# Kernel tuning notes

Measured on AMD Instinct MI355X. Metric: run time of the kernel, lower is better.

The kernel has to match this reference:

```python
import math
import jax, jax.numpy as jnp
import numpy as np

B, S, IN_DIM, D_MODEL, L, T_Y = 16, 512, 64, 64, 32, 256
T_X = T_Y + L - 1
RIDGE = 0.01
THRESH = 0.005


def _pos_encoding(seq_len, d):
    pos = jnp.arange(seq_len, dtype=jnp.float32)[:, None]
    div = jnp.exp(jnp.arange(0, d, 2, dtype=jnp.float32) * (-(math.log(10000.0) / d)))
    ang = pos * div  # [S, d/2]
    pe = jnp.zeros((seq_len, d), dtype=jnp.float32)
    pe = pe.at[:, 0::2].set(jnp.sin(ang)).at[:, 1::2].set(jnp.cos(ang))
    return pe


def _layernorm(h, gamma, beta, eps=1e-5):
    mu = jnp.mean(h, axis=-1, keepdims=True)
    var = jnp.mean((h - mu) ** 2, axis=-1, keepdims=True)
    return (h - mu) * jax.lax.rsqrt(var + eps) * gamma + beta


def setup_inputs() -> dict:
    key = jax.random.key(0)
    ks = jax.random.split(key, 8)
    return {
        "fps": jax.random.normal(ks[0], (B, S, IN_DIM), dtype=jnp.float32),
        "x": jax.random.normal(ks[1], (B, S, T_X), dtype=jnp.float32),
        "y": jax.random.normal(ks[2], (B, S, T_Y), dtype=jnp.float32),
        "sample_steps": jax.random.randint(ks[3], (5,), 10, S),
        "W1": jax.random.normal(ks[4], (IN_DIM, 256), dtype=jnp.float32) / math.sqrt(IN_DIM),
        "b1": jnp.zeros((256,), dtype=jnp.float32),
        "gamma": jnp.ones((256,), dtype=jnp.float32),
        "beta": jnp.zeros((256,), dtype=jnp.float32),
        "W2": jax.random.normal(ks[5], (256, D_MODEL), dtype=jnp.float32) / math.sqrt(256.0),
        "b2": jnp.zeros((D_MODEL,), dtype=jnp.float32),
        "Wq": jax.random.normal(ks[6], (D_MODEL, D_MODEL), dtype=jnp.float32) / math.sqrt(D_MODEL),
        "bq": jnp.zeros((D_MODEL,), dtype=jnp.float32),
        "Wk": jax.random.normal(ks[7], (D_MODEL, D_MODEL), dtype=jnp.float32) / math.sqrt(D_MODEL),
        "bk": jnp.zeros((D_MODEL,), dtype=jnp.float32),
    }


def reference(fps, x, y, sample_steps, W1, b1, gamma, beta, W2, b2, Wq, bq, Wk, bk):
    batch, seq_len, _ = fps.shape
    d = Wq.shape[0]
    t_y = y.shape[-1]
    filt = x.shape[-1] - t_y + 1  # L

    # encoder: Linear -> LayerNorm -> Tanh -> Linear -> Tanh
    h = _layernorm(fps @ W1 + b1, gamma, beta)
    e_orig = jnp.tanh(jnp.tanh(h) @ W2 + b2)  # [B,S,d]
    e = e_orig + 0.05 * _pos_encoding(seq_len, d)[None]

    q = e @ Wq + bq
    k = e @ Wk + bk
    scores = jnp.einsum('bsd,btd->bst', q, k) / math.sqrt(d)
    causal = jnp.triu(jnp.ones((seq_len, seq_len), dtype=bool), 1)
    scores = jnp.where(causal[None], -1e9, scores)
    alpha = jax.nn.softmax(scores * 2.0, axis=-1)  # [B,S,S]

    # sliding windows: X[b,s] = unfold(x[b,s], L, 1)[:T_y] -> [T_y, L]
    win = jnp.arange(t_y)[:, None] + jnp.arange(filt)[None, :]
    X = x[:, :, win]  # [B,S,T_y,L]

    # per-source gram / cross contributions
    G = jnp.einsum('bstl,bstm->bslm', X, X)  # [B,S,L,L]
    C = jnp.einsum('bstl,bst->bsl', X, y)    # [B,S,L]

    w = alpha[:, sample_steps, :]            # [B,T,S]
    wm = jnp.where(w > THRESH, w, 0.0)

    gram = jnp.einsum('bts,bslm->btlm', wm, G) + RIDGE * jnp.eye(filt, dtype=x.dtype)
    cross = jnp.einsum('bts,bsl->btl', wm, C)
    wt_hat = jnp.linalg.solve(gram, cross[..., None])[..., 0]  # [B,T,L]

    Xt = X[:, sample_steps]  # [B,T,T_y,L]
    yt = y[:, sample_steps]  # [B,T,T_y]
    pred = jnp.einsum('btkl,btl->btk', Xt, wt_hat)
    loss_bt = jnp.mean((yt - pred) ** 2, axis=-1)  # [B,T]

    valid = jnp.any(wm > 0.0, axis=-1)  # [B,T]
    total = jnp.sum(jnp.where(valid, loss_bt, 0.0))
    n = jnp.maximum(jnp.sum(valid.astype(jnp.int32)), 1)
    loss = total / n
    return loss, alpha, e_orig
```

## Files before the change

### kernel.cpp

```cpp
#include <hip/hip_runtime.h>
#include <hip/hip_bf16.h>
#include <math.h>

#define BB 16
#define SS 512
#define INDIM 64
#define DMODEL 64
#define HID 256
#define FILT 32
#define TYY 256
#define TXX 287
#define NT 5
#define RIDGEF 0.01f
#define THRESHF 0.005f

__global__ __launch_bounds__(256) void k_mlp(
    const float* __restrict__ fps, const float* __restrict__ W1, const float* __restrict__ b1,
    const float* __restrict__ gamma, const float* __restrict__ beta,
    const float* __restrict__ W2, const float* __restrict__ b2,
    const float* __restrict__ Wq, const float* __restrict__ bq,
    const float* __restrict__ Wk, const float* __restrict__ bk,
    float* __restrict__ e_out, float* __restrict__ q_out, float* __restrict__ kT_out)
{
    const int row0 = blockIdx.x << 2;
    const int tid = threadIdx.x;
    const int wid = tid >> 6, lane = tid & 63;

    __shared__ float fr[4][INDIM];
    __shared__ float th4[4][HID];
    __shared__ float ee4[4][DMODEL];
    __shared__ float part4[4][4][DMODEL];
    __shared__ float partk4[4][4][DMODEL];
    __shared__ float wred[4][4][2];

    { int r = tid >> 6, i = tid & 63;
      fr[r][i] = fps[(row0 + r) * INDIM + i]; }
    __syncthreads();

    float h[4];
    float b1v = b1[tid];
    #pragma unroll
    for (int r = 0; r < 4; ++r) h[r] = b1v;
    for (int i = 0; i < INDIM; ++i) {
        float w = W1[i * HID + tid];
        #pragma unroll
        for (int r = 0; r < 4; ++r) h[r] = fmaf(fr[r][i], w, h[r]);
    }

    float s1[4], s2[4];
    #pragma unroll
    for (int r = 0; r < 4; ++r) { s1[r] = h[r]; s2[r] = h[r] * h[r]; }
    #pragma unroll
    for (int off = 1; off < 64; off <<= 1) {
        #pragma unroll
        for (int r = 0; r < 4; ++r) {
            s1[r] += __shfl_xor(s1[r], off);
            s2[r] += __shfl_xor(s2[r], off);
        }
    }
    if (lane == 0) {
        #pragma unroll
        for (int r = 0; r < 4; ++r) { wred[wid][r][0] = s1[r]; wred[wid][r][1] = s2[r]; }
    }
    __syncthreads();
    float gm = gamma[tid], bt = beta[tid];
    #pragma unroll
    for (int r = 0; r < 4; ++r) {
        float t1 = wred[0][r][0] + wred[1][r][0] + wred[2][r][0] + wred[3][r][0];
        float t2 = wred[0][r][1] + wred[1][r][1] + wred[2][r][1] + wred[3][r][1];
        float mu = t1 * (1.0f / HID);
        float var = t2 * (1.0f / HID) - mu * mu;
        float hn = (h[r] - mu) * rsqrtf(var + 1e-5f) * gm + bt;
        th4[r][tid] = tanhf(hn);
    }
    __syncthreads();

    { int p = tid >> 6, j = tid & 63;
      float acc[4] = {0.f, 0.f, 0.f, 0.f};
      for (int i = p * 64; i < p * 64 + 64; ++i) {
          float w = W2[i * DMODEL + j];
          #pragma unroll
          for (int r = 0; r < 4; ++r) acc[r] = fmaf(th4[r][i], w, acc[r]);
      }
      #pragma unroll
      for (int r = 0; r < 4; ++r) part4[p][r][j] = acc[r];
    }
    __syncthreads();
    { int r = tid >> 6, j = tid & 63;
      float e = part4[0][r][j] + part4[1][r][j] + part4[2][r][j] + part4[3][r][j] + b2[j];
      float eo = tanhf(e);
      int row = row0 + r;
      int s = row & (SS - 1);
      e_out[(size_t)row * DMODEL + j] = eo;
      float div = expf(-(float)(j & ~1) * 0.14391156831212787f);
      float ang = (float)s * div;
      float pe = (j & 1) ? cosf(ang) : sinf(ang);
      ee4[r][j] = eo + 0.05f * pe;
    }
    __syncthreads();
    { int p = tid >> 6, j = tid & 63;
      float aq[4] = {0.f,0.f,0.f,0.f}, ak[4] = {0.f,0.f,0.f,0.f};
      for (int i = p * 16; i < p * 16 + 16; ++i) {
          float wqv = Wq[i * DMODEL + j];
          float wkv = Wk[i * DMODEL + j];
          #pragma unroll
          for (int r = 0; r < 4; ++r) {
              aq[r] = fmaf(ee4[r][i], wqv, aq[r]);
              ak[r] = fmaf(ee4[r][i], wkv, ak[r]);
          }
      }
      #pragma unroll
      for (int r = 0; r < 4; ++r) { part4[p][r][j] = aq[r]; partk4[p][r][j] = ak[r]; }
    }
    __syncthreads();
    { int r = tid >> 6, j = tid & 63;
      float qv = part4[0][r][j] + part4[1][r][j] + part4[2][r][j] + part4[3][r][j] + bq[j];
      float kv = partk4[0][r][j] + partk4[1][r][j] + partk4[2][r][j] + partk4[3][r][j] + bk[j];
      int row = row0 + r;
      int b = row >> 9, s = row & (SS - 1);
      q_out[(size_t)row * DMODEL + j] = qv;
      kT_out[(size_t)(b * DMODEL + j) * SS + s] = kv;
    }
}

__global__ __launch_bounds__(256) void k_attn(
    const float* __restrict__ q, const float* __restrict__ kT,
    float* __restrict__ alpha)
{
    const int blk = blockIdx.x;
    const int b = blk >> 7;
    const int t0 = (blk & 127) << 2;
    const int t3 = t0 + 3;
    const int tid = threadIdx.x;
    const int wave = tid >> 6, lane = tid & 63;

    __shared__ float qt[4 * DMODEL];
    __shared__ float redm[4][4];

    qt[tid] = q[(size_t)(b * SS + t0 + (tid >> 6)) * DMODEL + (tid & 63)];
    __syncthreads();

    const float* kTb = kT + (size_t)b * DMODEL * SS;
    const int s0 = tid, s1 = tid + 256;
    float a0[4] = {0,0,0,0}, a1[4] = {0,0,0,0};
    if (s1 <= t3) {
        for (int d = 0; d < DMODEL; ++d) {
            float k0 = kTb[d * SS + s0];
            float k1 = kTb[d * SS + s1];
            #pragma unroll
            for (int r = 0; r < 4; ++r) {
                float qv = qt[r * DMODEL + d];
                a0[r] = fmaf(qv, k0, a0[r]);
                a1[r] = fmaf(qv, k1, a1[r]);
            }
        }
    } else if (s0 <= t3) {
        for (int d = 0; d < DMODEL; ++d) {
            float k0 = kTb[d * SS + s0];
            #pragma unroll
            for (int r = 0; r < 4; ++r) a0[r] = fmaf(qt[r * DMODEL + d], k0, a0[r]);
        }
    }
    float lg0[4], lg1[4];
    #pragma unroll
    for (int r = 0; r < 4; ++r) {
        int tr = t0 + r;
        lg0[r] = (s0 <= tr) ? 0.25f * a0[r] : -INFINITY;
        lg1[r] = (s1 <= tr) ? 0.25f * a1[r] : -INFINITY;
    }
    float mr[4];
    #pragma unroll
    for (int r = 0; r < 4; ++r) {
        float m = fmaxf(lg0[r], lg1[r]);
        #pragma unroll
        for (int off = 32; off > 0; off >>= 1) m = fmaxf(m, __shfl_xor(m, off));
        if (lane == 0) redm[r][wave] = m;
    }
    __syncthreads();
    #pragma unroll
    for (int r = 0; r < 4; ++r)
        mr[r] = fmaxf(fmaxf(redm[r][0], redm[r][1]), fmaxf(redm[r][2], redm[r][3]));
    __syncthreads();
    float ex0[4], ex1[4], sr[4];
    #pragma unroll
    for (int r = 0; r < 4; ++r) {
        ex0[r] = expf(lg0[r] - mr[r]);
        ex1[r] = expf(lg1[r] - mr[r]);
        float sm = ex0[r] + ex1[r];
        #pragma unroll
        for (int off = 32; off > 0; off >>= 1) sm += __shfl_xor(sm, off);
        if (lane == 0) redm[r][wave] = sm;
    }
    __syncthreads();
    #pragma unroll
    for (int r = 0; r < 4; ++r)
        sr[r] = redm[r][0] + redm[r][1] + redm[r][2] + redm[r][3];
    #pragma unroll
    for (int r = 0; r < 4; ++r) {
        float inv = 1.0f / sr[r];
        size_t base = (size_t)(b * SS + t0 + r) * SS;
        alpha[base + s0] = ex0[r] * inv;
        alpha[base + s1] = ex1[r] * inv;
    }
}

__global__ __launch_bounds__(256) void k_gpart(
    const float* __restrict__ x, const float* __restrict__ y,
    const int* __restrict__ steps, const float* __restrict__ alpha,
    float* __restrict__ part, int C, int CS)
{
    const int b = blockIdx.x / C;
    const int chunk = blockIdx.x % C;
    const int tid = threadIdx.x;
    const int lane = tid & 63, wid = tid >> 6;

    __shared__ __align__(16) float xs[288];
    __shared__ __align__(16) float ys[256];
    __shared__ float Gs[1056];
    __shared__ float crossL[32];
    __shared__ float wv[NT * 64];
    __shared__ int sl[64];
    __shared__ int nselS;
    __shared__ int stS[NT];
    __shared__ float redA[4][33];
    __shared__ float redB[4][33];

    if (tid < NT) stS[tid] = steps[tid];
    if (tid < 32) Gs[tid * 33 + 32] = 0.f;
    __syncthreads();

    for (int idx = tid; idx < NT * CS; idx += 256) {
        int t = idx / CS, si = idx % CS;
        float a = alpha[(size_t)(b * SS + stS[t]) * SS + chunk * CS + si];
        wv[t * 64 + si] = (a > THRESHF) ? a : 0.f;
    }
    __syncthreads();
    if (tid == 0) {
        int c = 0;
        for (int si = 0; si < CS; ++si) {
            float m = wv[si] + wv[64 + si] + wv[128 + si] + wv[192 + si] + wv[256 + si];
            if (m > 0.f) sl[c++] = si;
        }
        nselS = c;
    }
    __syncthreads();
    const int nsel = nselS;

    float acc[NT][5];
    #pragma unroll
    for (int t = 0; t < NT; ++t) {
        #pragma unroll
        for (int r = 0; r < 5; ++r) acc[t][r] = 0.f;
    }

    float rx0 = 0.f, rx1 = 0.f, ry = 0.f;
    if (nsel > 0) {
        int sg = chunk * CS + sl[0];
        const float* xr = x + (size_t)(b * SS + sg) * TXX;
        const float* yr = y + (size_t)(b * SS + sg) * TYY;
        rx0 = xr[tid];
        if (tid < 31) rx1 = xr[256 + tid];
        ry = yr[tid];
    }

    for (int i = 0; i < nsel; ++i) {
        xs[tid] = rx0;
        if (tid < 31) xs[256 + tid] = rx1;
        ys[tid] = ry;
        const int sl_cur = sl[i];
        __syncthreads();

        if (i + 1 < nsel) {
            int sg = chunk * CS + sl[i + 1];
            const float* xr = x + (size_t)(b * SS + sg) * TXX;
            const float* yr = y + (size_t)(b * SS + sg) * TYY;
            rx0 = xr[tid];
            if (tid < 31) rx1 = xr[256 + tid];
            ry = yr[tid];
        }

        { int l = tid & 31, p = tid >> 5;
          const float4* xk4 = (const float4*)(xs + (p << 5));
          const float4* yk4 = (const float4*)(ys + (p << 5));
          float c = 0.f, a = 0.f;
          #pragma unroll
          for (int j = 0; j < 8; ++j) {
              float4 xk = xk4[j];
              float4 yk = yk4[j];
              int kb = (p << 5) + (j << 2);
              float x0 = xs[kb + l],     x1 = xs[kb + 1 + l];
              float x2 = xs[kb + 2 + l], x3 = xs[kb + 3 + l];
              c = fmaf(x0, yk.x, c); a = fmaf(xk.x, x0, a);
              c = fmaf(x1, yk.y, c); a = fmaf(xk.y, x1, a);
              c = fmaf(x2, yk.z, c); a = fmaf(xk.z, x2, a);
              c = fmaf(x3, yk.w, c); a = fmaf(xk.w, x3, a);
          }
          c += __shfl_xor(c, 32);
          a += __shfl_xor(a, 32);
          if (lane < 32) { redA[wid][l] = c; redB[wid][l] = a; }
        }
        __syncthreads();

        if (tid < 32)
            crossL[tid] = redA[0][tid] + redA[1][tid] + redA[2][tid] + redA[3][tid];

        { int jj = lane & 31;
          #pragma unroll
          for (int pass = 0; pass < 4; ++pass) {
              int dd = 2 * (wid + 4 * pass) + (lane >> 5);
              float g0 = redB[0][dd] + redB[1][dd] + redB[2][dd] + redB[3][dd];
              float dlt = 0.f;
              if (jj > 0 && jj + dd < 32)
                  dlt = xs[jj + 255] * xs[jj + 255 + dd]
                      - xs[jj - 1] * xs[jj - 1 + dd];
              #pragma unroll
              for (int off = 1; off < 32; off <<= 1) {
                  float tsh = __shfl_up(dlt, off, 32);
                  if (jj >= off) dlt += tsh;
              }
              if (jj + dd < 32) {
                  float gval = g0 + dlt;
                  Gs[jj * 33 + jj + dd] = gval;
                  Gs[(jj + dd) * 33 + jj] = gval;
              }
          }
        }
        __syncthreads();

        { float g0 = Gs[tid], g1 = Gs[tid + 256], g2 = Gs[tid + 512], g3 = Gs[tid + 768];
          float g4 = (tid < 32) ? Gs[1024 + tid]
                   : ((tid < 64) ? crossL[tid - 32] : 0.f);
          #pragma unroll
          for (int t = 0; t < NT; ++t) {
              float w = wv[t * 64 + sl_cur];
              if (w > 0.f) {
                  acc[t][0] = fmaf(w, g0, acc[t][0]);
                  acc[t][1] = fmaf(w, g1, acc[t][1]);
                  acc[t][2] = fmaf(w, g2, acc[t][2]);
                  acc[t][3] = fmaf(w, g3, acc[t][3]);
                  acc[t][4] = fmaf(w, g4, acc[t][4]);
              }
          }
        }
    }

    #pragma unroll
    for (int t = 0; t < NT; ++t) {
        size_t base = (size_t)((b * NT + t) * C + chunk) * 1088;
        #pragma unroll
        for (int r = 0; r < 4; ++r) part[base + tid + 256 * r] = acc[t][r];
        if (tid < 64) part[base + 1024 + tid] = acc[t][4];
    }
}

__global__ __launch_bounds__(256) void k_solve2(
    const float* __restrict__ x, const float* __restrict__ y,
    const int* __restrict__ steps, const float* __restrict__ alpha,
    const float* __restrict__ part,
    float* __restrict__ lossbt, int* __restrict__ valid, int C)
{
    const int g = blockIdx.x;
    const int b = g / NT, t = g % NT;
    const int tid = threadIdx.x;

    __shared__ float Af[1056];
    __shared__ float zs[FILT];
    __shared__ float wt[FILT];
    __shared__ float xsr[TXX + 1];
    __shared__ float red[256];
    __shared__ int step_s;
    __shared__ int anyv;

    if (tid == 0) { step_s = steps[t]; anyv = 0; }
    __syncthreads();

    float a0 = 0.f, a1 = 0.f, a2 = 0.f, a3 = 0.f, a4 = 0.f;
    for (int ch = 0; ch < C; ++ch) {
        const float* pp = part + (size_t)(g * C + ch) * 1088;
        a0 += pp[tid];
        a1 += pp[tid + 256];
        a2 += pp[tid + 512];
        a3 += pp[tid + 768];
        if (tid < 64) a4 += pp[tid + 1024];
    }
    Af[tid] = a0; Af[tid + 256] = a1; Af[tid + 512] = a2; Af[tid + 768] = a3;
    if (tid < 32) Af[1024 + tid] = a4;
    else if (tid < 64) zs[tid - 32] = a4;

    { const float* arow = alpha + (size_t)(b * SS + step_s) * SS;
      if (arow[tid] > THRESHF || arow[tid + 256] > THRESHF) anyv = 1; }
    __syncthreads();
    if (tid < 32) Af[tid * 33 + tid] += RIDGEF;
    __syncthreads();

    if (tid < 32) {
        float a[32];
        #pragma unroll
        for (int j = 0; j < 32; ++j) a[j] = Af[tid * 33 + j];
        #pragma unroll
        for (int k = 0; k < 32; ++k) {
            float akk = __shfl(a[k], k);
            float dk = sqrtf(akk);
            float ck = a[k] / dk;
            if (tid >= k) a[k] = ck;
            #pragma unroll
            for (int m = k + 1; m < 32; ++m) {
                float cm = __shfl(ck, m);
                if (tid >= m) a[m] = fmaf(-ck, cm, a[m]);
            }
        }
        #pragma unroll
        for (int j = 0; j < 32; ++j)
            if (j <= tid) Af[tid * 33 + j] = a[j];

        float zl = zs[tid];
        #pragma unroll
        for (int k = 0; k < 32; ++k) {
            float akk = __shfl(a[k], k);
            float zk = __shfl(zl, k) / akk;
            if (tid == k) zl = zk;
            else if (tid > k) zl = fmaf(-a[k], zk, zl);
        }
        #pragma unroll
        for (int k = 31; k >= 0; --k) {
            float akk = __shfl(a[k], k);
            float wk = __shfl(zl, k) / akk;
            if (tid == k) zl = wk;
            else if (tid < k) zl = fmaf(-Af[k * 33 + tid], wk, zl);
        }
        wt[tid] = zl;
    }
    __syncthreads();

    const int sstep = step_s;
    const float* xrow = x + (size_t)(b * SS + sstep) * TXX;
    for (int i = tid; i < TXX; i += 256) xsr[i] = xrow[i];
    __syncthreads();
    float pk = 0.f;
    #pragma unroll
    for (int l = 0; l < FILT; ++l) pk = fmaf(xsr[tid + l], wt[l], pk);
    float d = y[(size_t)(b * SS + sstep) * TYY + tid] - pk;
    red[tid] = d * d;
    __syncthreads();
    for (int off = 128; off > 0; off >>= 1) {
        if (tid < off) red[tid] += red[tid + off];
        __syncthreads();
    }
    if (tid == 0) {
        lossbt[g] = red[0] * (1.0f / TYY);
        valid[g] = anyv;
    }
}

__global__ __launch_bounds__(128) void k_final(
    const float* __restrict__ lossbt, const int* __restrict__ valid,
    float* __restrict__ out0)
{
    __shared__ float rs[128];
    __shared__ int rc[128];
    int tid = threadIdx.x;
    float v = 0.f; int c = 0;
    if (tid < BB * NT && valid[tid]) { v = lossbt[tid]; c = 1; }
    rs[tid] = v; rc[tid] = c;
    __syncthreads();
    for (int off = 64; off > 0; off >>= 1) {
        if (tid < off) { rs[tid] += rs[tid + off]; rc[tid] += rc[tid + off]; }
        __syncthreads();
    }
    if (tid == 0) {
        int n = rc[0] > 0 ? rc[0] : 1;
        out0[0] = rs[0] / (float)n;
    }
}

extern "C" void kernel_launch(void* const* d_in, const int* in_sizes, int n_in,
                              void* d_out, int out_size, void* d_ws, size_t ws_size,
                              hipStream_t stream)
{
    const float* fps  = (const float*)d_in[0];
    const float* x    = (const float*)d_in[1];
    const float* y    = (const float*)d_in[2];
    const int* steps  = (const int*)d_in[3];
    const float* W1   = (const float*)d_in[4];
    const float* b1   = (const float*)d_in[5];
    const float* gamma= (const float*)d_in[6];
    const float* beta = (const float*)d_in[7];
    const float* W2   = (const float*)d_in[8];
    const float* b2   = (const float*)d_in[9];
    const float* Wq   = (const float*)d_in[10];
    const float* bq   = (const float*)d_in[11];
    const float* Wk   = (const float*)d_in[12];
    const float* bk   = (const float*)d_in[13];

    float* out   = (float*)d_out;
    float* alpha = out + 1;
    float* e_out = out + 1 + (size_t)BB * SS * SS;

    float* lossbt = (float*)d_ws;
    int*   valid  = (int*)(lossbt + 128);
    float* shreg  = (float*)d_ws + 256;
    float* q      = shreg;
    float* kT     = q + (size_t)BB * SS * DMODEL;
    float* part   = shreg;

    size_t avail_f = (ws_size > 1024) ? (ws_size / 4 - 256) : 0;
    int C = 64;
    while (C > 8 && (size_t)(BB * NT) * C * 1088 > avail_f) C >>= 1;
    int CS = SS / C;

    hipLaunchKernelGGL(k_mlp, dim3(BB * SS / 4), dim3(256), 0, stream,
                       fps, W1, b1, gamma, beta, W2, b2, Wq, bq, Wk, bk,
                       e_out, q, kT);
    hipLaunchKernelGGL(k_attn, dim3(BB * (SS / 4)), dim3(256), 0, stream,
                       q, kT, alpha);
    hipLaunchKernelGGL(k_gpart, dim3(BB * C), dim3(256), 0, stream,
                       x, y, steps, alpha, part, C, CS);
    hipLaunchKernelGGL(k_solve2, dim3(BB * NT), dim3(256), 0, stream,
                       x, y, steps, alpha, part, lossbt, valid, C);
    hipLaunchKernelGGL(k_final, dim3(1), dim3(128), 0, stream, lossbt, valid, out);
}
```

Before: 209.9 us.

## Split chunk reduction into parallel kernel and process 8 rows per MLP block

Adds a k_reduce kernel that sums the per-chunk gram/cross partials across 400 blocks into a compact gram buffer. Previously the 80 k_solve2 blocks each did this summation serially. k_mlp now handles 8 rows per block, reusing each W1 load across more rows and halving the block count; the second-layer and projection stages run in two halves of 4 rows. The changes add a kernel launch, an extra workspace buffer, and more registers in k_mlp.

```diff
diff --git a/kernel.cpp b/kernel.cpp
--- a/kernel.cpp
+++ b/kernel.cpp
@@ -22,50 +22,51 @@
     const float* __restrict__ Wk, const float* __restrict__ bk,
     float* __restrict__ e_out, float* __restrict__ q_out, float* __restrict__ kT_out)
 {
-    const int row0 = blockIdx.x << 2;
+    const int row0 = blockIdx.x << 3;
     const int tid = threadIdx.x;
     const int wid = tid >> 6, lane = tid & 63;
 
-    __shared__ float fr[4][INDIM];
-    __shared__ float th4[4][HID];
+    __shared__ float fr[8][INDIM];
+    __shared__ float th4[8][HID];
     __shared__ float ee4[4][DMODEL];
     __shared__ float part4[4][4][DMODEL];
     __shared__ float partk4[4][4][DMODEL];
-    __shared__ float wred[4][4][2];
+    __shared__ float wred[4][8][2];
 
     { int r = tid >> 6, i = tid & 63;
-      fr[r][i] = fps[(row0 + r) * INDIM + i]; }
-    __syncthreads();
-
-    float h[4];
+      fr[r][i]     = fps[(row0 + r) * INDIM + i];
+      fr[r + 4][i] = fps[(row0 + r + 4) * INDIM + i]; }
+    __syncthreads();
+
+    float h[8];
     float b1v = b1[tid];
     #pragma unroll
-    for (int r = 0; r < 4; ++r) h[r] = b1v;
+    for (int r = 0; r < 8; ++r) h[r] = b1v;
     for (int i = 0; i < INDIM; ++i) {
         float w = W1[i * HID + tid];
         #pragma unroll
-        for (int r = 0; r < 4; ++r) h[r] = fmaf(fr[r][i], w, h[r]);
-    }
-
-    float s1[4], s2[4];
-    #pragma unroll
-    for (int r = 0; r < 4; ++r) { s1[r] = h[r]; s2[r] = h[r] * h[r]; }
+        for (int r = 0; r < 8; ++r) h[r] = fmaf(fr[r][i], w, h[r]);
+    }
+
+    float s1[8], s2[8];
+    #pragma unroll
+    for (int r = 0; r < 8; ++r) { s1[r] = h[r]; s2[r] = h[r] * h[r]; }
     #pragma unroll
     for (int off = 1; off < 64; off <<= 1) {
         #pragma unroll
-        for (int r = 0; r < 4; ++r) {
+        for (int r = 0; r < 8; ++r) {
             s1[r] += __shfl_xor(s1[r], off);
             s2[r] += __shfl_xor(s2[r], off);
         }
     }
     if (lane == 0) {
         #pragma unroll
-        for (int r = 0; r < 4; ++r) { wred[wid][r][0] = s1[r]; wred[wid][r][1] = s2[r]; }
+        for (int r = 0; r < 8; ++r) { wred[wid][r][0] = s1[r]; wred[wid][r][1] = s2[r]; }
     }
     __syncthreads();
     float gm = gamma[tid], bt = beta[tid];
     #pragma unroll
-    for (int r = 0; r < 4; ++r) {
+    for (int r = 0; r < 8; ++r) {
         float t1 = wred[0][r][0] + wred[1][r][0] + wred[2][r][0] + wred[3][r][0];
         float t2 = wred[0][r][1] + wred[1][r][1] + wred[2][r][1] + wred[3][r][1];
         float mu = t1 * (1.0f / HID);
@@ -75,51 +76,56 @@
     }
     __syncthreads();
 
-    { int p = tid >> 6, j = tid & 63;
-      float acc[4] = {0.f, 0.f, 0.f, 0.f};
-      for (int i = p * 64; i < p * 64 + 64; ++i) {
-          float w = W2[i * DMODEL + j];
+    #pragma unroll
+    for (int half = 0; half < 2; ++half) {
+        const int rbase = half * 4;
+        { int p = tid >> 6, j = tid & 63;
+          float acc[4] = {0.f, 0.f, 0.f, 0.f};
+          for (int i = p * 64; i < p * 64 + 64; ++i) {
+              float w = W2[i * DMODEL + j];
+              #pragma unroll
+              for (int r = 0; r < 4; ++r) acc[r] = fmaf(th4[rbase + r][i], w, acc[r]);
+          }
           #pragma unroll
-          for (int r = 0; r < 4; ++r) acc[r] = fmaf(th4[r][i], w, acc[r]);
-      }
-      #pragma unroll
-      for (int r = 0; r < 4; ++r) part4[p][r][j] = acc[r];
-    }
-    __syncthreads();
-    { int r = tid >> 6, j = tid & 63;
-      float e = part4[0][r][j] + part4[1][r][j] + part4[2][r][j] + part4[3][r][j] + b2[j];
-      float eo = tanhf(e);
-      int row = row0 + r;
-      int s = row & (SS - 1);
-      e_out[(size_t)row * DMODEL + j] = eo;
-      float div = expf(-(float)(j & ~1) * 0.14391156831212787f);
-      float ang = (float)s * div;
-      float pe = (j & 1) ? cosf(ang) : sinf(ang);
-      ee4[r][j] = eo + 0.05f * pe;
-    }
-    __syncthreads();
-    { int p = tid >> 6, j = tid & 63;
-      float aq[4] = {0.f,0.f,0.f,0.f}, ak[4] = {0.f,0.f,0.f,0.f};
-      for (int i = p * 16; i < p * 16 + 16; ++i) {
-          float wqv = Wq[i * DMODEL + j];
-          float wkv = Wk[i * DMODEL + j];
+          for (int r = 0; r < 4; ++r) part4[p][r][j] = acc[r];
+        }
+        __syncthreads();
+        { int r = tid >> 6, j = tid & 63;
+          float e = part4[0][r][j] + part4[1][r][j] + part4[2][r][j] + part4[3][r][j] + b2[j];
+          float eo = tanhf(e);
+          int row = row0 + rbase + r;
+          int s = row & (SS - 1);
+          e_out[(size_t)row * DMODEL + j] = eo;
+          float div = expf(-(float)(j & ~1) * 0.14391156831212787f);
+          float ang = (float)s * div;
+          float pe = (j & 1) ? cosf(ang) : sinf(ang);
+          ee4[r][j] = eo + 0.05f * pe;
+        }
+        __syncthreads();
+        { int p = tid >> 6, j = tid & 63;
+          float aq[4] = {0.f,0.f,0.f,0.f}, ak[4] = {0.f,0.f,0.f,0.f};
+          for (int i = p * 16; i < p * 16 + 16; ++i) {
+              float wqv = Wq[i * DMODEL + j];
+              float wkv = Wk[i * DMODEL + j];
+              #pragma unroll
+              for (int r = 0; r < 4; ++r) {
+                  aq[r] = fmaf(ee4[r][i], wqv, aq[r]);
+                  ak[r] = fmaf(ee4[r][i], wkv, ak[r]);
+              }
+          }
           #pragma unroll
-          for (int r = 0; r < 4; ++r) {
-              aq[r] = fmaf(ee4[r][i], wqv, aq[r]);
-              ak[r] = fmaf(ee4[r][i], wkv, ak[r]);
-          }
-      }
-      #pragma unroll
-      for (int r = 0; r < 4; ++r) { part4[p][r][j] = aq[r]; partk4[p][r][j] = ak[r]; }
-    }
-    __syncthreads();
-    { int r = tid >> 6, j = tid & 63;
-      float qv = part4[0][r][j] + part4[1][r][j] + part4[2][r][j] + part4[3][r][j] + bq[j];
-      float kv = partk4[0][r][j] + partk4[1][r][j] + partk4[2][r][j] + partk4[3][r][j] + bk[j];
-      int row = row0 + r;
-      int b = row >> 9, s = row & (SS - 1);
-      q_out[(size_t)row * DMODEL + j] = qv;
-      kT_out[(size_t)(b * DMODEL + j) * SS + s] = kv;
+          for (int r = 0; r < 4; ++r) { part4[p][r][j] = aq[r]; partk4[p][r][j] = ak[r]; }
+        }
+        __syncthreads();
+        { int r = tid >> 6, j = tid & 63;
+          float qv = part4[0][r][j] + part4[1][r][j] + part4[2][r][j] + part4[3][r][j] + bq[j];
+          float kv = partk4[0][r][j] + partk4[1][r][j] + partk4[2][r][j] + partk4[3][r][j] + bk[j];
+          int row = row0 + rbase + r;
+          int b = row >> 9, s = row & (SS - 1);
+          q_out[(size_t)row * DMODEL + j] = qv;
+          kT_out[(size_t)(b * DMODEL + j) * SS + s] = kv;
+        }
+        __syncthreads();
     }
 }
 
@@ -353,11 +359,33 @@
     }
 }
 
+__global__ __launch_bounds__(256) void k_reduce(
+    const float* __restrict__ part, float* __restrict__ gram, int C)
+{
+    const int g = blockIdx.x / 5;
+    const int seg = blockIdx.x % 5;
+    const int tid = threadIdx.x;
+    int idx = seg * 256 + tid;
+    if (idx >= 1088) return;
+
+    const float* pp = part + (size_t)g * C * 1088 + idx;
+    float s0 = 0.f, s1 = 0.f, s2 = 0.f, s3 = 0.f;
+    int ch = 0;
+    for (; ch + 4 <= C; ch += 4) {
+        s0 += pp[(size_t)(ch + 0) * 1088];
+        s1 += pp[(size_t)(ch + 1) * 1088];
+        s2 += pp[(size_t)(ch + 2) * 1088];
+        s3 += pp[(size_t)(ch + 3) * 1088];
+    }
+    for (; ch < C; ++ch) s0 += pp[(size_t)ch * 1088];
+    gram[(size_t)g * 1088 + idx] = (s0 + s1) + (s2 + s3);
+}
+
 __global__ __launch_bounds__(256) void k_solve2(
     const float* __restrict__ x, const float* __restrict__ y,
     const int* __restrict__ steps, const float* __restrict__ alpha,
-    const float* __restrict__ part,
-    float* __restrict__ lossbt, int* __restrict__ valid, int C)
+    const float* __restrict__ gram,
+    float* __restrict__ lossbt, int* __restrict__ valid)
 {
     const int g = blockIdx.x;
     const int b = g / NT, t = g % NT;
@@ -374,18 +402,13 @@
     if (tid == 0) { step_s = steps[t]; anyv = 0; }
     __syncthreads();
 
-    float a0 = 0.f, a1 = 0.f, a2 = 0.f, a3 = 0.f, a4 = 0.f;
-    for (int ch = 0; ch < C; ++ch) {
-        const float* pp = part + (size_t)(g * C + ch) * 1088;
-        a0 += pp[tid];
-        a1 += pp[tid + 256];
-        a2 += pp[tid + 512];
-        a3 += pp[tid + 768];
-        if (tid < 64) a4 += pp[tid + 1024];
-    }
-    Af[tid] = a0; Af[tid + 256] = a1; Af[tid + 512] = a2; Af[tid + 768] = a3;
-    if (tid < 32) Af[1024 + tid] = a4;
-    else if (tid < 64) zs[tid - 32] = a4;
+    const float* row = gram + (size_t)g * 1088;
+    Af[tid] = row[tid];
+    Af[tid + 256] = row[tid + 256];
+    Af[tid + 512] = row[tid + 512];
+    Af[tid + 768] = row[tid + 768];
+    if (tid < 32) Af[1024 + tid] = row[1024 + tid];
+    else if (tid < 64) zs[tid - 32] = row[1024 + tid];
 
     { const float* arow = alpha + (size_t)(b * SS + step_s) * SS;
       if (arow[tid] > THRESHF || arow[tid + 256] > THRESHF) anyv = 1; }
@@ -498,24 +521,28 @@
 
     float* lossbt = (float*)d_ws;
     int*   valid  = (int*)(lossbt + 128);
-    float* shreg  = (float*)d_ws + 256;
+    float* gram   = (float*)d_ws + 256;
+    float* shreg  = gram + (size_t)BB * NT * 1088;
     float* q      = shreg;
     float* kT     = q + (size_t)BB * SS * DMODEL;
     float* part   = shreg;
 
-    size_t avail_f = (ws_size > 1024) ? (ws_size / 4 - 256) : 0;
+    size_t head_f = 256 + (size_t)BB * NT * 1088;
+    size_t avail_f = (ws_size / 4 > head_f) ? (ws_size / 4 - head_f) : 0;
     int C = 64;
     while (C > 8 && (size_t)(BB * NT) * C * 1088 > avail_f) C >>= 1;
     int CS = SS / C;
 
-    hipLaunchKernelGGL(k_mlp, dim3(BB * SS / 4), dim3(256), 0, stream,
+    hipLaunchKernelGGL(k_mlp, dim3(BB * SS / 8), dim3(256), 0, stream,
                        fps, W1, b1, gamma, beta, W2, b2, Wq, bq, Wk, bk,
                        e_out, q, kT);
     hipLaunchKernelGGL(k_attn, dim3(BB * (SS / 4)), dim3(256), 0, stream,
                        q, kT, alpha);
     hipLaunchKernelGGL(k_gpart, dim3(BB * C), dim3(256), 0, stream,
                        x, y, steps, alpha, part, C, CS);
+    hipLaunchKernelGGL(k_reduce, dim3(BB * NT * 5), dim3(256), 0, stream,
+                       part, gram, C);
     hipLaunchKernelGGL(k_solve2, dim3(BB * NT), dim3(256), 0, stream,
-                       x, y, steps, alpha, part, lossbt, valid, C);
+                       x, y, steps, alpha, gram, lossbt, valid);
     hipLaunchKernelGGL(k_final, dim3(1), dim3(128), 0, stream, lossbt, valid, out);
 }
```

Result: no change. 208.6 us (-0.6%).
